# Kernel optimization log

Hardware: AMD Instinct MI355X
Metric: run time of the kernel (lower is better)

## Reference

```python
import jax, jax.numpy as jnp
import numpy as np

C = 512
B, H, W = 4, 64, 64
GROUPS = 32
EPS = 1e-6
SCALE = 1.0 / np.sqrt(C)


def setup_inputs() -> dict:
    key = jax.random.key(0)
    ks = jax.random.split(key, 3)
    x = jax.random.normal(ks[0], (B, C, H, W), dtype=jnp.float32)
    # conv weights: kaiming-ish small init for numerical sanity
    qkv_w = jax.random.normal(ks[1], (3 * C, C), dtype=jnp.float32) * (1.0 / np.sqrt(C))
    proj_w = jax.random.normal(ks[2], (C, C), dtype=jnp.float32) * (1.0 / np.sqrt(C))
    return {
        "x": x,
        "norm_w": jnp.ones((C,), jnp.float32),
        "norm_b": jnp.zeros((C,), jnp.float32),
        "qkv_w": qkv_w,
        "qkv_b": jnp.zeros((3 * C,), jnp.float32),
        "proj_w": proj_w,
        "proj_b": jnp.zeros((C,), jnp.float32),
    }


def reference(x, norm_w, norm_b, qkv_w, qkv_b, proj_w, proj_b):
    b, c, h, w = x.shape
    hw = h * w
    # GroupNorm(32, eps=1e-6, affine)
    xg = x.reshape(b, GROUPS, -1)                       # [B, G, (C/G)*H*W]
    mean = jnp.mean(xg, axis=-1, keepdims=True)
    var = jnp.var(xg, axis=-1, keepdims=True)
    xn = ((xg - mean) * jax.lax.rsqrt(var + EPS)).reshape(b, c, h, w)
    xn = xn * norm_w[:, None, None] + norm_b[:, None, None]
    # 1x1 conv qkv == channel matmul
    qkv = jnp.einsum('oc,bchw->bohw', qkv_w, xn) + qkv_b[:, None, None]
    q, k, v = jnp.split(qkv, 3, axis=1)                 # each [B, C, H, W]
    q = q.reshape(b, c, hw)                              # [B, C, HW]
    k = k.reshape(b, c, hw)
    v = v.reshape(b, c, hw)
    # attn[b, i, j] = softmax_j( q_i . k_j * scale )
    scores = jnp.einsum('bci,bcj->bij', q, k) * SCALE    # [B, HW, HW]
    attn = jax.nn.softmax(scores, axis=-1)
    # h[b, c, i] = sum_j v[b, c, j] * attn[b, i, j]
    hmap = jnp.einsum('bcj,bij->bci', v, attn).reshape(b, c, h, w)
    out = x + jnp.einsum('oc,bchw->bohw', proj_w, hmap) + proj_b[:, None, None]
    return out
```

## Files before the change

kernel.cpp:

```cpp
#include <hip/hip_runtime.h>
#include <hip/hip_fp8.h>
#include <cstdint>
#include <cmath>

#define B_   4
#define C_   512
#define HW_  4096
#define G_   32
#define CPG_ 16
#define EPS_ 1e-6f
#define SCALE_ 0.04419417382415922f
#define PSCALE_ 0.0625f


typedef __bf16 bf16_t;
typedef __bf16 bf16x8 __attribute__((ext_vector_type(8)));
typedef __bf16 bf16x4 __attribute__((ext_vector_type(4)));
typedef float  f32x4  __attribute__((ext_vector_type(4)));
typedef int    i32x4  __attribute__((ext_vector_type(4)));
typedef int    i32x8  __attribute__((ext_vector_type(8)));
typedef unsigned int u32;
typedef __hip_fp8_e4m3 fp8_t;

__device__ __forceinline__ void cp16(const void* g, void* l) {
  __builtin_amdgcn_global_load_lds((__attribute__((address_space(1))) u32*)(g),
                                   (__attribute__((address_space(3))) u32*)(l),
                                   16, 0, 0);
}

__device__ __forceinline__ void zero_acc(f32x4 acc[4][4]) {
  f32x4 z = {0.f, 0.f, 0.f, 0.f};
#pragma unroll
  for (int i = 0; i < 4; ++i)
#pragma unroll
    for (int j = 0; j < 4; ++j) acc[i][j] = z;
}

__device__ __forceinline__ void gemm_bt64(const bf16_t* __restrict__ A,
                                          const bf16_t* __restrict__ B,
                                          int K, int lda, int ldb,
                                          f32x4 acc[4][4]) {
  __shared__ __align__(16) bf16_t As[128 * 64];
  __shared__ __align__(16) bf16_t Bs[128 * 64];
  const int tid  = threadIdx.x;
  const int wave = tid >> 6;
  const int lane = tid & 63;
  const int wm = (wave >> 1) * 64;
  const int wn = (wave & 1) * 64;
  const int srow = lane >> 3;
  const int gch  = ((lane & 7) - srow) & 7;
  const bf16_t* gA = A + (size_t)(wave * 32 + srow) * lda + gch * 8;
  const bf16_t* gB = B + (size_t)(wave * 32 + srow) * ldb + gch * 8;
  bf16_t* lA = As + wave * 32 * 64;
  bf16_t* lB = Bs + wave * 32 * 64;
  const int fr = lane & 15;
  const int q  = lane >> 4;
  const int eo0 = ((q + fr) & 7) * 8;
  const int eo1 = ((q + 4 + fr) & 7) * 8;

  for (int k0 = 0; k0 < K; k0 += 64) {
#pragma unroll
    for (int cc = 0; cc < 4; ++cc) {
      cp16(gA + (size_t)(cc * 8) * lda, lA + cc * 512);
      cp16(gB + (size_t)(cc * 8) * ldb, lB + cc * 512);
    }
    gA += 64; gB += 64;
    __syncthreads();
#pragma unroll
    for (int h = 0; h < 2; ++h) {
      const int eo = h ? eo1 : eo0;
      bf16x8 a[4], b[4];
#pragma unroll
      for (int i = 0; i < 4; ++i)
        a[i] = *(const bf16x8*)(As + (wm + i * 16 + fr) * 64 + eo);
#pragma unroll
      for (int j = 0; j < 4; ++j)
        b[j] = *(const bf16x8*)(Bs + (wn + j * 16 + fr) * 64 + eo);
#pragma unroll
      for (int i = 0; i < 4; ++i)
#pragma unroll
        for (int j = 0; j < 4; ++j)
          acc[i][j] = __builtin_amdgcn_mfma_f32_16x16x32_bf16(a[i], b[j], acc[i][j], 0, 0, 0);
    }
    __syncthreads();
  }
}

template <bool ROWSUM>
__device__ __forceinline__ void gemm_bt_mx(const unsigned char* __restrict__ A,
                                           const unsigned char* __restrict__ B,
                                           int K, int lda, int ldb,
                                           f32x4 acc[4][4], f32x4 accl[4]) {
  __shared__ __align__(16) unsigned char As[128 * 128];
  __shared__ __align__(16) unsigned char Bs[128 * 128];
  const int tid  = threadIdx.x;
  const int wave = tid >> 6;
  const int lane = tid & 63;
  const int wm = (wave >> 1) * 64;
  const int wn = (wave & 1) * 64;
  const int srow = lane >> 3;
  const int gch  = ((lane & 7) - srow) & 7;
  const unsigned char* gA = A + (size_t)(wave * 32 + srow) * lda + gch * 16;
  const unsigned char* gB = B + (size_t)(wave * 32 + srow) * ldb + gch * 16;
  unsigned char* lA = As + wave * 32 * 128;
  unsigned char* lB = Bs + wave * 32 * 128;
  const int fr = lane & 15;
  const int q  = lane >> 4;
  const int co0 = ((2 * q     + fr) & 7) * 16;
  const int co1 = ((2 * q + 1 + fr) & 7) * 16;
  const i32x8 vones = {0x38383838, 0x38383838, 0x38383838, 0x38383838,
                       0x38383838, 0x38383838, 0x38383838, 0x38383838};

  for (int k0 = 0; k0 < K; k0 += 128) {
#pragma unroll
    for (int cc = 0; cc < 4; ++cc) {
      cp16(gA + (size_t)(cc * 8) * lda, lA + cc * 1024);
      cp16(gB + (size_t)(cc * 8) * ldb, lB + cc * 1024);
    }
    gA += 128; gB += 128;
    __syncthreads();
    i32x8 a[4], b[4];
#pragma unroll
    for (int i = 0; i < 4; ++i) {
      const int ro = (wm + i * 16 + fr) * 128;
      i32x4 lo = *(const i32x4*)(As + ro + co0);
      i32x4 hi = *(const i32x4*)(As + ro + co1);
      a[i] = __builtin_shufflevector(lo, hi, 0, 1, 2, 3, 4, 5, 6, 7);
    }
#pragma unroll
    for (int j = 0; j < 4; ++j) {
      const int ro = (wn + j * 16 + fr) * 128;
      i32x4 lo = *(const i32x4*)(Bs + ro + co0);
      i32x4 hi = *(const i32x4*)(Bs + ro + co1);
      b[j] = __builtin_shufflevector(lo, hi, 0, 1, 2, 3, 4, 5, 6, 7);
    }
#pragma unroll
    for (int i = 0; i < 4; ++i) {
#pragma unroll
      for (int j = 0; j < 4; ++j)
        acc[i][j] = __builtin_amdgcn_mfma_scale_f32_16x16x128_f8f6f4(
            a[i], b[j], acc[i][j], 0, 0, 0, 0x7F, 0, 0x7F);
      if (ROWSUM)
        accl[i] = __builtin_amdgcn_mfma_scale_f32_16x16x128_f8f6f4(
            a[i], vones, accl[i], 0, 0, 0, 0x7F, 0, 0x7F);
    }
    __syncthreads();
  }
}


__global__ void __launch_bounds__(256) cast_w_kernel(const float* __restrict__ qkv_w,
                                                     const float* __restrict__ proj_w,
                                                     bf16_t* __restrict__ wqkv,
                                                     bf16_t* __restrict__ wproj) {
  int idx = blockIdx.x * 256 + threadIdx.x;
  const int nq = 1536 * 512;
  if (idx < nq) {
    wqkv[idx] = (bf16_t)qkv_w[idx];
  } else {
    int t = idx - nq;
    int p = t & 511;
    int off = p & 63;
    int c = (p & ~63) + ((off & 3) << 4) + (off >> 2);
    wproj[t] = (bf16_t)proj_w[(t & ~511) + c];
  }
}

__global__ void __launch_bounds__(256) gn_partial_kernel(const float* __restrict__ x,
                                                         float* __restrict__ stats) {
  __shared__ float rs[256], rss[256];
  const int bg = blockIdx.x >> 3;
  const int ch = blockIdx.x & 7;
  const float4* base = (const float4*)(x + (size_t)bg * (CPG_ * HW_)) +
                       (size_t)ch * (CPG_ * HW_ / 4 / 8);
  float s = 0.f, ss = 0.f;
  for (int i = threadIdx.x; i < CPG_ * HW_ / 4 / 8; i += 256) {
    float4 v = base[i];
    s  += v.x + v.y + v.z + v.w;
    ss += v.x * v.x + v.y * v.y + v.z * v.z + v.w * v.w;
  }
  rs[threadIdx.x] = s; rss[threadIdx.x] = ss;
  __syncthreads();
  for (int st = 128; st > 0; st >>= 1) {
    if ((int)threadIdx.x < st) {
      rs[threadIdx.x]  += rs[threadIdx.x + st];
      rss[threadIdx.x] += rss[threadIdx.x + st];
    }
    __syncthreads();
  }
  if (threadIdx.x == 0) {
    atomicAdd(&stats[bg * 2 + 0], rs[0]);
    atomicAdd(&stats[bg * 2 + 1], rss[0]);
  }
}

__global__ void __launch_bounds__(256) norm_tr_kernel(const float* __restrict__ x,
                                                      const float* __restrict__ stats,
                                                      const float* __restrict__ nw,
                                                      const float* __restrict__ nb,
                                                      bf16_t* __restrict__ xnT) {
  __shared__ float tile[64][65];
  const int b  = blockIdx.z;
  const int i0 = blockIdx.x * 64;
  const int c0 = blockIdx.y * 64;
  const int tx = threadIdx.x & 63;
  const int ty = threadIdx.x >> 6;
  const int cbase = c0 + ty * 16;
  const int g = cbase >> 4;
  const float inv = 1.f / (float)(CPG_ * HW_);
  const float sum  = stats[(b * G_ + g) * 2 + 0];
  const float ssum = stats[(b * G_ + g) * 2 + 1];
  const float mean = sum * inv;
  const float rstd = rsqrtf(ssum * inv - mean * mean + EPS_);
#pragma unroll
  for (int r = 0; r < 16; ++r) {
    const int c = cbase + r;
    float v = x[((size_t)b * C_ + c) * HW_ + i0 + tx];
    tile[ty * 16 + r][tx] = (v - mean) * rstd * nw[c] + nb[c];
  }
  __syncthreads();
#pragma unroll
  for (int r = 0; r < 16; ++r) {
    const int il = ty * 16 + r;
    xnT[((size_t)b * HW_ + i0 + il) * C_ + c0 + tx] = (bf16_t)tile[tx][il];
  }
}


__global__ void __launch_bounds__(256) qk_gemm_kernel(const bf16_t* __restrict__ xnT,
                                                      const bf16_t* __restrict__ wqkv,
                                                      const float* __restrict__ qkv_b,
                                                      fp8_t* __restrict__ QKt8) {
  const int b = blockIdx.z;
  f32x4 acc[4][4]; zero_acc(acc);
  const bf16_t* A  = xnT + ((size_t)b * HW_ + blockIdx.y * 128) * C_;
  const bf16_t* Bp = wqkv + (size_t)blockIdx.x * 128 * C_;
  gemm_bt64(A, Bp, C_, C_, C_, acc);
  const int lane = threadIdx.x & 63, wave = threadIdx.x >> 6;
  const int wm = (wave >> 1) * 64, wn = (wave & 1) * 64;
  const int fr = lane & 15, q = lane >> 4;
  const int r0 = blockIdx.y * 128 + wm + (q << 2);
  const int cb = blockIdx.x * 128 + wn;
  float bias[4];
#pragma unroll
  for (int j = 0; j < 4; ++j) bias[j] = qkv_b[cb + fr + j * 16];
#pragma unroll
  for (int i = 0; i < 4; ++i)
#pragma unroll
    for (int r = 0; r < 4; ++r) {
      const int row = r0 + i * 16 + r;
      u32 dw = 0;
      dw = (u32)__builtin_amdgcn_cvt_pk_fp8_f32(acc[i][0][r] + bias[0],
                                                acc[i][1][r] + bias[1], (int)dw, false);
      dw = (u32)__builtin_amdgcn_cvt_pk_fp8_f32(acc[i][2][r] + bias[2],
                                                acc[i][3][r] + bias[3], (int)dw, true);
      *(u32*)((unsigned char*)QKt8 + ((size_t)b * HW_ + row) * 1024 + cb + fr * 4) = dw;
    }
}

__global__ void __launch_bounds__(256) v_gemm_kernel(const bf16_t* __restrict__ wqkv,
                                                     const bf16_t* __restrict__ xnT,
                                                     const float* __restrict__ qkv_b,
                                                     fp8_t* __restrict__ V8) {
  const int b = blockIdx.z;
  f32x4 acc[4][4]; zero_acc(acc);
  const bf16_t* A  = wqkv + (size_t)(1024 + blockIdx.y * 128) * C_;
  const bf16_t* Bp = xnT + ((size_t)b * HW_ + blockIdx.x * 128) * C_;
  gemm_bt64(A, Bp, C_, C_, C_, acc);
  const int lane = threadIdx.x & 63, wave = threadIdx.x >> 6;
  const int wm = (wave >> 1) * 64, wn = (wave & 1) * 64;
  const int fr = lane & 15, q = lane >> 4;
  const int r0 = blockIdx.y * 128 + wm + (q << 2);
  const int cb = blockIdx.x * 128 + wn;
#pragma unroll
  for (int i = 0; i < 4; ++i)
#pragma unroll
    for (int r = 0; r < 4; ++r) {
      const int row = r0 + i * 16 + r;
      const float bias = qkv_b[1024 + row];
      u32 dw = 0;
      dw = (u32)__builtin_amdgcn_cvt_pk_fp8_f32(acc[i][0][r] + bias,
                                                acc[i][1][r] + bias, (int)dw, false);
      dw = (u32)__builtin_amdgcn_cvt_pk_fp8_f32(acc[i][2][r] + bias,
                                                acc[i][3][r] + bias, (int)dw, true);
      *(u32*)((unsigned char*)V8 + ((size_t)b * C_ + row) * HW_ + cb + fr * 4) = dw;
    }
}

__global__ void __launch_bounds__(256) sexp_gemm_kernel(const fp8_t* __restrict__ QKt8,
                                                        fp8_t* __restrict__ P8) {
  const int n   = blockIdx.x;
  const int xcd = n & 7;
  const int p   = n >> 3;
  const int xb  = p & 31;
  const int grp = xcd * 16 + (p >> 5);
  const int yb  = grp & 31;
  const int b   = grp >> 5;

  const unsigned char* QKtb = (const unsigned char*)QKt8 + (size_t)b * HW_ * 1024;
  fp8_t* Pb = P8 + (size_t)b * HW_ * HW_;
  f32x4 acc[4][4]; zero_acc(acc);
  const unsigned char* A  = QKtb + (size_t)yb * 128 * 1024;
  const unsigned char* Bp = QKtb + 512 + (size_t)xb * 128 * 1024;
  gemm_bt_mx<false>(A, Bp, 512, 1024, 1024, acc, nullptr);
  const int lane = threadIdx.x & 63, wave = threadIdx.x >> 6;
  const int wm = (wave >> 1) * 64, wn = (wave & 1) * 64;
  const int fr = lane & 15, q = lane >> 4;
  const int r0 = yb * 128 + wm + (q << 2);
  const int cb = xb * 128 + wn;
#pragma unroll
  for (int i = 0; i < 4; ++i)
#pragma unroll
    for (int r = 0; r < 4; ++r) {
      const int row = r0 + i * 16 + r;
      float e0 = __expf(acc[i][0][r] * SCALE_) * PSCALE_;
      float e1 = __expf(acc[i][1][r] * SCALE_) * PSCALE_;
      float e2 = __expf(acc[i][2][r] * SCALE_) * PSCALE_;
      float e3 = __expf(acc[i][3][r] * SCALE_) * PSCALE_;
      u32 dw = 0;
      dw = (u32)__builtin_amdgcn_cvt_pk_fp8_f32(e0, e1, (int)dw, false);
      dw = (u32)__builtin_amdgcn_cvt_pk_fp8_f32(e2, e3, (int)dw, true);
      *(u32*)((unsigned char*)Pb + (size_t)row * HW_ + cb + fr * 4) = dw;
    }
}

__global__ void __launch_bounds__(256) pv_gemm_kernel(const fp8_t* __restrict__ P8,
                                                      const fp8_t* __restrict__ V8,
                                                      bf16_t* __restrict__ hmT) {
  const int n   = blockIdx.x;
  const int xcd = n & 7;
  const int p   = n >> 3;
  const int xb  = p & 3;
  const int grp = xcd * 16 + (p >> 2);
  const int yb  = grp & 31;
  const int b   = grp >> 5;

  const unsigned char* A  = (const unsigned char*)P8 + (size_t)b * HW_ * HW_ +
                            (size_t)yb * 128 * HW_;
  const unsigned char* Bp = (const unsigned char*)V8 + (size_t)b * C_ * HW_ +
                            (size_t)xb * 128 * HW_;
  bf16_t* hmTb = hmT + (size_t)b * HW_ * C_;

  f32x4 acc[4][4]; zero_acc(acc);
  f32x4 accl[4];
  {
    f32x4 z = {0.f, 0.f, 0.f, 0.f};
#pragma unroll
    for (int i = 0; i < 4; ++i) accl[i] = z;
  }
  gemm_bt_mx<true>(A, Bp, HW_, HW_, HW_, acc, accl);

  const int lane = threadIdx.x & 63, wave = threadIdx.x >> 6;
  const int wm = (wave >> 1) * 64, wn = (wave & 1) * 64;
  const int fr = lane & 15, q = lane >> 4;
  const int r0 = yb * 128 + wm + (q << 2);
  const int cb = xb * 128 + wn;
#pragma unroll
  for (int i = 0; i < 4; ++i)
#pragma unroll
    for (int r = 0; r < 4; ++r) {
      const int row = r0 + i * 16 + r;
      const float rl = 1.f / accl[i][r];
      bf16x4 o;
#pragma unroll
      for (int j = 0; j < 4; ++j) o[j] = (bf16_t)(acc[i][j][r] * rl);
      *(bf16x4*)(hmTb + (size_t)row * C_ + cb + fr * 4) = o;
    }
}

__global__ void __launch_bounds__(256) proj_gemm_kernel(const bf16_t* __restrict__ wproj,
                                                        const bf16_t* __restrict__ hmT,
                                                        const float* __restrict__ proj_b,
                                                        const float* __restrict__ x,
                                                        float* __restrict__ out) {
  const int b = blockIdx.z;
  f32x4 acc[4][4]; zero_acc(acc);
  const bf16_t* A  = wproj + (size_t)blockIdx.y * 128 * C_;
  const bf16_t* Bp = hmT + ((size_t)b * HW_ + blockIdx.x * 128) * C_;
  gemm_bt64(A, Bp, C_, C_, C_, acc);
  const int lane = threadIdx.x & 63, wave = threadIdx.x >> 6;
  const int wm = (wave >> 1) * 64, wn = (wave & 1) * 64;
  const int r0 = blockIdx.y * 128 + wm + ((lane >> 4) << 2);
  const int c0 = blockIdx.x * 128 + wn + (lane & 15);
#pragma unroll
  for (int i = 0; i < 4; ++i)
#pragma unroll
    for (int r = 0; r < 4; ++r) {
      const int row = r0 + i * 16 + r;
      const float bias = proj_b[row];
#pragma unroll
      for (int j = 0; j < 4; ++j) {
        const int col = c0 + j * 16;
        const size_t idx = ((size_t)b * C_ + row) * HW_ + col;
        out[idx] = x[idx] + bias + acc[i][j][r];
      }
    }
}

extern "C" void kernel_launch(void* const* d_in, const int* in_sizes, int n_in,
                              void* d_out, int out_size, void* d_ws, size_t ws_size,
                              hipStream_t stream) {
  const float* x      = (const float*)d_in[0];
  const float* norm_w = (const float*)d_in[1];
  const float* norm_b = (const float*)d_in[2];
  const float* qkv_w  = (const float*)d_in[3];
  const float* qkv_b  = (const float*)d_in[4];
  const float* proj_w = (const float*)d_in[5];
  const float* proj_b = (const float*)d_in[6];
  float* out = (float*)d_out;

  char* ws = (char*)d_ws;
  size_t o = 0;
  bf16_t* wqkv  = (bf16_t*)(ws + o); o += (size_t)1536 * 512 * 2;
  bf16_t* wproj = (bf16_t*)(ws + o); o += (size_t)512 * 512 * 2;
  float*  stats = (float*)(ws + o);  o += 128 * 2 * 4;
  bf16_t* xnT   = (bf16_t*)(ws + o); o += (size_t)B_ * HW_ * C_ * 2;
  fp8_t*  QKt8  = (fp8_t*)(ws + o);  o += (size_t)B_ * HW_ * 1024;
  fp8_t*  V8    = (fp8_t*)(ws + o);  o += (size_t)B_ * C_ * HW_;
  bf16_t* hmT   = (bf16_t*)(ws + o); o += (size_t)B_ * HW_ * C_ * 2;
  fp8_t*  P8    = (fp8_t*)(ws + o);  o += (size_t)B_ * HW_ * HW_;

  cast_w_kernel<<<4096, 256, 0, stream>>>(qkv_w, proj_w, wqkv, wproj);
  hipMemsetAsync(stats, 0, 128 * 2 * sizeof(float), stream);
  gn_partial_kernel<<<1024, 256, 0, stream>>>(x, stats);
  norm_tr_kernel<<<dim3(HW_ / 64, C_ / 64, B_), 256, 0, stream>>>(x, stats, norm_w, norm_b, xnT);
  qk_gemm_kernel<<<dim3(1024 / 128, HW_ / 128, B_), 256, 0, stream>>>(xnT, wqkv, qkv_b, QKt8);
  v_gemm_kernel<<<dim3(HW_ / 128, C_ / 128, B_), 256, 0, stream>>>(wqkv, xnT, qkv_b, V8);
  sexp_gemm_kernel<<<4096, 256, 0, stream>>>(QKt8, P8);
  pv_gemm_kernel<<<512, 256, 0, stream>>>(P8, V8, hmT);
  proj_gemm_kernel<<<dim3(HW_ / 128, C_ / 128, B_), 256, 0, stream>>>(
      wproj, hmT, proj_b, x, out);
}
```

Before: 247.8 us.

## Convert QKV, V and projection GEMMs from bf16 to scaled fp8 MFMA

Weights, the normalized input and the attention output are now stored as fp8 e4m3 instead of bf16. Weights and hmap are pre-scaled by 16, and the MFMA scale exponents (0x7B) undo that factor. The three 512-deep GEMMs (QK, V, proj) now use the fp8 scaled MFMA path instead of bf16 MFMA, which halves their global and LDS traffic and doubles MFMA throughput. The cost is lower precision in the projections and the residual-path GEMM, which may hurt accuracy.

```diff
diff --git a/kernel.cpp b/kernel.cpp
--- a/kernel.cpp
+++ b/kernel.cpp
@@ -15,7 +15,6 @@
 
 typedef __bf16 bf16_t;
 typedef __bf16 bf16x8 __attribute__((ext_vector_type(8)));
-typedef __bf16 bf16x4 __attribute__((ext_vector_type(4)));
 typedef float  f32x4  __attribute__((ext_vector_type(4)));
 typedef int    i32x4  __attribute__((ext_vector_type(4)));
 typedef int    i32x8  __attribute__((ext_vector_type(8)));
@@ -36,57 +35,7 @@
     for (int j = 0; j < 4; ++j) acc[i][j] = z;
 }
 
-__device__ __forceinline__ void gemm_bt64(const bf16_t* __restrict__ A,
-                                          const bf16_t* __restrict__ B,
-                                          int K, int lda, int ldb,
-                                          f32x4 acc[4][4]) {
-  __shared__ __align__(16) bf16_t As[128 * 64];
-  __shared__ __align__(16) bf16_t Bs[128 * 64];
-  const int tid  = threadIdx.x;
-  const int wave = tid >> 6;
-  const int lane = tid & 63;
-  const int wm = (wave >> 1) * 64;
-  const int wn = (wave & 1) * 64;
-  const int srow = lane >> 3;
-  const int gch  = ((lane & 7) - srow) & 7;
-  const bf16_t* gA = A + (size_t)(wave * 32 + srow) * lda + gch * 8;
-  const bf16_t* gB = B + (size_t)(wave * 32 + srow) * ldb + gch * 8;
-  bf16_t* lA = As + wave * 32 * 64;
-  bf16_t* lB = Bs + wave * 32 * 64;
-  const int fr = lane & 15;
-  const int q  = lane >> 4;
-  const int eo0 = ((q + fr) & 7) * 8;
-  const int eo1 = ((q + 4 + fr) & 7) * 8;
-
-  for (int k0 = 0; k0 < K; k0 += 64) {
-#pragma unroll
-    for (int cc = 0; cc < 4; ++cc) {
-      cp16(gA + (size_t)(cc * 8) * lda, lA + cc * 512);
-      cp16(gB + (size_t)(cc * 8) * ldb, lB + cc * 512);
-    }
-    gA += 64; gB += 64;
-    __syncthreads();
-#pragma unroll
-    for (int h = 0; h < 2; ++h) {
-      const int eo = h ? eo1 : eo0;
-      bf16x8 a[4], b[4];
-#pragma unroll
-      for (int i = 0; i < 4; ++i)
-        a[i] = *(const bf16x8*)(As + (wm + i * 16 + fr) * 64 + eo);
-#pragma unroll
-      for (int j = 0; j < 4; ++j)
-        b[j] = *(const bf16x8*)(Bs + (wn + j * 16 + fr) * 64 + eo);
-#pragma unroll
-      for (int i = 0; i < 4; ++i)
-#pragma unroll
-        for (int j = 0; j < 4; ++j)
-          acc[i][j] = __builtin_amdgcn_mfma_f32_16x16x32_bf16(a[i], b[j], acc[i][j], 0, 0, 0);
-    }
-    __syncthreads();
-  }
-}
-
-template <bool ROWSUM>
+template <bool ROWSUM, int SA = 0x7F, int SB = 0x7F>
 __device__ __forceinline__ void gemm_bt_mx(const unsigned char* __restrict__ A,
                                            const unsigned char* __restrict__ B,
                                            int K, int lda, int ldb,
@@ -139,10 +88,10 @@
 #pragma unroll
       for (int j = 0; j < 4; ++j)
         acc[i][j] = __builtin_amdgcn_mfma_scale_f32_16x16x128_f8f6f4(
-            a[i], b[j], acc[i][j], 0, 0, 0, 0x7F, 0, 0x7F);
+            a[i], b[j], acc[i][j], 0, 0, 0, SA, 0, SB);
       if (ROWSUM)
         accl[i] = __builtin_amdgcn_mfma_scale_f32_16x16x128_f8f6f4(
-            a[i], vones, accl[i], 0, 0, 0, 0x7F, 0, 0x7F);
+            a[i], vones, accl[i], 0, 0, 0, SA, 0, 0x7F);
     }
     __syncthreads();
   }
@@ -151,18 +100,32 @@
 
 __global__ void __launch_bounds__(256) cast_w_kernel(const float* __restrict__ qkv_w,
                                                      const float* __restrict__ proj_w,
-                                                     bf16_t* __restrict__ wqkv,
-                                                     bf16_t* __restrict__ wproj) {
-  int idx = blockIdx.x * 256 + threadIdx.x;
+                                                     fp8_t* __restrict__ wqkv8,
+                                                     fp8_t* __restrict__ wproj8) {
+  const int idx = blockIdx.x * 256 + threadIdx.x;
+  const int t = idx * 4;
   const int nq = 1536 * 512;
-  if (idx < nq) {
-    wqkv[idx] = (bf16_t)qkv_w[idx];
+  if (t < nq) {
+    u32 dw = 0;
+    dw = (u32)__builtin_amdgcn_cvt_pk_fp8_f32(qkv_w[t] * 16.f, qkv_w[t + 1] * 16.f, (int)dw, false);
+    dw = (u32)__builtin_amdgcn_cvt_pk_fp8_f32(qkv_w[t + 2] * 16.f, qkv_w[t + 3] * 16.f, (int)dw, true);
+    *(u32*)((unsigned char*)wqkv8 + t) = dw;
   } else {
-    int t = idx - nq;
-    int p = t & 511;
-    int off = p & 63;
-    int c = (p & ~63) + ((off & 3) << 4) + (off >> 2);
-    wproj[t] = (bf16_t)proj_w[(t & ~511) + c];
+    const int tt = t - nq;
+    const int o = tt >> 9;
+    const int p = tt & 511;
+    float v[4];
+#pragma unroll
+    for (int e = 0; e < 4; ++e) {
+      const int pe = p + e;
+      const int off = pe & 63;
+      const int c = (pe & ~63) + ((off & 3) << 4) + (off >> 2);
+      v[e] = proj_w[(o << 9) + c] * 16.f;
+    }
+    u32 dw = 0;
+    dw = (u32)__builtin_amdgcn_cvt_pk_fp8_f32(v[0], v[1], (int)dw, false);
+    dw = (u32)__builtin_amdgcn_cvt_pk_fp8_f32(v[2], v[3], (int)dw, true);
+    *(u32*)((unsigned char*)wproj8 + tt) = dw;
   }
 }
 
@@ -198,7 +161,7 @@
                                                       const float* __restrict__ stats,
                                                       const float* __restrict__ nw,
                                                       const float* __restrict__ nb,
-                                                      bf16_t* __restrict__ xnT) {
+                                                      fp8_t* __restrict__ xnT8) {
   __shared__ float tile[64][65];
   const int b  = blockIdx.z;
   const int i0 = blockIdx.x * 64;
@@ -219,23 +182,28 @@
     tile[ty * 16 + r][tx] = (v - mean) * rstd * nw[c] + nb[c];
   }
   __syncthreads();
-#pragma unroll
-  for (int r = 0; r < 16; ++r) {
-    const int il = ty * 16 + r;
-    xnT[((size_t)b * HW_ + i0 + il) * C_ + c0 + tx] = (bf16_t)tile[tx][il];
-  }
-}
-
-
-__global__ void __launch_bounds__(256) qk_gemm_kernel(const bf16_t* __restrict__ xnT,
-                                                      const bf16_t* __restrict__ wqkv,
+  const int il = threadIdx.x >> 2;
+  const int q4 = threadIdx.x & 3;
+#pragma unroll
+  for (int m = 0; m < 4; ++m) {
+    const int cq = q4 + m * 4;
+    u32 dw = 0;
+    dw = (u32)__builtin_amdgcn_cvt_pk_fp8_f32(tile[cq * 4 + 0][il], tile[cq * 4 + 1][il], (int)dw, false);
+    dw = (u32)__builtin_amdgcn_cvt_pk_fp8_f32(tile[cq * 4 + 2][il], tile[cq * 4 + 3][il], (int)dw, true);
+    *(u32*)((unsigned char*)xnT8 + ((size_t)b * HW_ + i0 + il) * C_ + c0 + cq * 4) = dw;
+  }
+}
+
+
+__global__ void __launch_bounds__(256) qk_gemm_kernel(const fp8_t* __restrict__ xnT8,
+                                                      const fp8_t* __restrict__ wqkv8,
                                                       const float* __restrict__ qkv_b,
                                                       fp8_t* __restrict__ QKt8) {
   const int b = blockIdx.z;
   f32x4 acc[4][4]; zero_acc(acc);
-  const bf16_t* A  = xnT + ((size_t)b * HW_ + blockIdx.y * 128) * C_;
-  const bf16_t* Bp = wqkv + (size_t)blockIdx.x * 128 * C_;
-  gemm_bt64(A, Bp, C_, C_, C_, acc);
+  const unsigned char* A  = (const unsigned char*)xnT8 + ((size_t)b * HW_ + blockIdx.y * 128) * C_;
+  const unsigned char* Bp = (const unsigned char*)wqkv8 + (size_t)blockIdx.x * 128 * C_;
+  gemm_bt_mx<false, 0x7F, 0x7B>(A, Bp, C_, C_, C_, acc, nullptr);
   const int lane = threadIdx.x & 63, wave = threadIdx.x >> 6;
   const int wm = (wave >> 1) * 64, wn = (wave & 1) * 64;
   const int fr = lane & 15, q = lane >> 4;
@@ -258,15 +226,15 @@
     }
 }
 
-__global__ void __launch_bounds__(256) v_gemm_kernel(const bf16_t* __restrict__ wqkv,
-                                                     const bf16_t* __restrict__ xnT,
+__global__ void __launch_bounds__(256) v_gemm_kernel(const fp8_t* __restrict__ wqkv8,
+                                                     const fp8_t* __restrict__ xnT8,
                                                      const float* __restrict__ qkv_b,
                                                      fp8_t* __restrict__ V8) {
   const int b = blockIdx.z;
   f32x4 acc[4][4]; zero_acc(acc);
-  const bf16_t* A  = wqkv + (size_t)(1024 + blockIdx.y * 128) * C_;
-  const bf16_t* Bp = xnT + ((size_t)b * HW_ + blockIdx.x * 128) * C_;
-  gemm_bt64(A, Bp, C_, C_, C_, acc);
+  const unsigned char* A  = (const unsigned char*)wqkv8 + (size_t)(1024 + blockIdx.y * 128) * C_;
+  const unsigned char* Bp = (const unsigned char*)xnT8 + ((size_t)b * HW_ + blockIdx.x * 128) * C_;
+  gemm_bt_mx<false, 0x7B, 0x7F>(A, Bp, C_, C_, C_, acc, nullptr);
   const int lane = threadIdx.x & 63, wave = threadIdx.x >> 6;
   const int wm = (wave >> 1) * 64, wn = (wave & 1) * 64;
   const int fr = lane & 15, q = lane >> 4;
@@ -326,7 +294,7 @@
 
 __global__ void __launch_bounds__(256) pv_gemm_kernel(const fp8_t* __restrict__ P8,
                                                       const fp8_t* __restrict__ V8,
-                                                      bf16_t* __restrict__ hmT) {
+                                                      fp8_t* __restrict__ hmT8) {
   const int n   = blockIdx.x;
   const int xcd = n & 7;
   const int p   = n >> 3;
@@ -339,7 +307,7 @@
                             (size_t)yb * 128 * HW_;
   const unsigned char* Bp = (const unsigned char*)V8 + (size_t)b * C_ * HW_ +
                             (size_t)xb * 128 * HW_;
-  bf16_t* hmTb = hmT + (size_t)b * HW_ * C_;
+  fp8_t* hmTb = hmT8 + (size_t)b * HW_ * C_;
 
   f32x4 acc[4][4]; zero_acc(acc);
   f32x4 accl[4];
@@ -360,24 +328,24 @@
 #pragma unroll
     for (int r = 0; r < 4; ++r) {
       const int row = r0 + i * 16 + r;
-      const float rl = 1.f / accl[i][r];
-      bf16x4 o;
-#pragma unroll
-      for (int j = 0; j < 4; ++j) o[j] = (bf16_t)(acc[i][j][r] * rl);
-      *(bf16x4*)(hmTb + (size_t)row * C_ + cb + fr * 4) = o;
-    }
-}
-
-__global__ void __launch_bounds__(256) proj_gemm_kernel(const bf16_t* __restrict__ wproj,
-                                                        const bf16_t* __restrict__ hmT,
+      const float rl = 16.f / accl[i][r];
+      u32 dw = 0;
+      dw = (u32)__builtin_amdgcn_cvt_pk_fp8_f32(acc[i][0][r] * rl, acc[i][1][r] * rl, (int)dw, false);
+      dw = (u32)__builtin_amdgcn_cvt_pk_fp8_f32(acc[i][2][r] * rl, acc[i][3][r] * rl, (int)dw, true);
+      *(u32*)((unsigned char*)hmTb + (size_t)row * C_ + cb + fr * 4) = dw;
+    }
+}
+
+__global__ void __launch_bounds__(256) proj_gemm_kernel(const fp8_t* __restrict__ wproj8,
+                                                        const fp8_t* __restrict__ hmT8,
                                                         const float* __restrict__ proj_b,
                                                         const float* __restrict__ x,
                                                         float* __restrict__ out) {
   const int b = blockIdx.z;
   f32x4 acc[4][4]; zero_acc(acc);
-  const bf16_t* A  = wproj + (size_t)blockIdx.y * 128 * C_;
-  const bf16_t* Bp = hmT + ((size_t)b * HW_ + blockIdx.x * 128) * C_;
-  gemm_bt64(A, Bp, C_, C_, C_, acc);
+  const unsigned char* A  = (const unsigned char*)wproj8 + (size_t)blockIdx.y * 128 * C_;
+  const unsigned char* Bp = (const unsigned char*)hmT8 + ((size_t)b * HW_ + blockIdx.x * 128) * C_;
+  gemm_bt_mx<false, 0x7B, 0x7B>(A, Bp, C_, C_, C_, acc, nullptr);
   const int lane = threadIdx.x & 63, wave = threadIdx.x >> 6;
   const int wm = (wave >> 1) * 64, wn = (wave & 1) * 64;
   const int r0 = blockIdx.y * 128 + wm + ((lane >> 4) << 2);
@@ -411,23 +379,23 @@
 
   char* ws = (char*)d_ws;
   size_t o = 0;
-  bf16_t* wqkv  = (bf16_t*)(ws + o); o += (size_t)1536 * 512 * 2;
-  bf16_t* wproj = (bf16_t*)(ws + o); o += (size_t)512 * 512 * 2;
-  float*  stats = (float*)(ws + o);  o += 128 * 2 * 4;
-  bf16_t* xnT   = (bf16_t*)(ws + o); o += (size_t)B_ * HW_ * C_ * 2;
-  fp8_t*  QKt8  = (fp8_t*)(ws + o);  o += (size_t)B_ * HW_ * 1024;
-  fp8_t*  V8    = (fp8_t*)(ws + o);  o += (size_t)B_ * C_ * HW_;
-  bf16_t* hmT   = (bf16_t*)(ws + o); o += (size_t)B_ * HW_ * C_ * 2;
-  fp8_t*  P8    = (fp8_t*)(ws + o);  o += (size_t)B_ * HW_ * HW_;
-
-  cast_w_kernel<<<4096, 256, 0, stream>>>(qkv_w, proj_w, wqkv, wproj);
+  fp8_t* wqkv8  = (fp8_t*)(ws + o); o += (size_t)1536 * 512;
+  fp8_t* wproj8 = (fp8_t*)(ws + o); o += (size_t)512 * 512;
+  float* stats  = (float*)(ws + o); o += 128 * 2 * 4;
+  fp8_t* xnT8   = (fp8_t*)(ws + o); o += (size_t)B_ * HW_ * C_;
+  fp8_t* QKt8   = (fp8_t*)(ws + o); o += (size_t)B_ * HW_ * 1024;
+  fp8_t* V8     = (fp8_t*)(ws + o); o += (size_t)B_ * C_ * HW_;
+  fp8_t* hmT8   = (fp8_t*)(ws + o); o += (size_t)B_ * HW_ * C_;
+  fp8_t* P8     = (fp8_t*)(ws + o); o += (size_t)B_ * HW_ * HW_;
+
+  cast_w_kernel<<<1024, 256, 0, stream>>>(qkv_w, proj_w, wqkv8, wproj8);
   hipMemsetAsync(stats, 0, 128 * 2 * sizeof(float), stream);
   gn_partial_kernel<<<1024, 256, 0, stream>>>(x, stats);
-  norm_tr_kernel<<<dim3(HW_ / 64, C_ / 64, B_), 256, 0, stream>>>(x, stats, norm_w, norm_b, xnT);
-  qk_gemm_kernel<<<dim3(1024 / 128, HW_ / 128, B_), 256, 0, stream>>>(xnT, wqkv, qkv_b, QKt8);
-  v_gemm_kernel<<<dim3(HW_ / 128, C_ / 128, B_), 256, 0, stream>>>(wqkv, xnT, qkv_b, V8);
+  norm_tr_kernel<<<dim3(HW_ / 64, C_ / 64, B_), 256, 0, stream>>>(x, stats, norm_w, norm_b, xnT8);
+  qk_gemm_kernel<<<dim3(1024 / 128, HW_ / 128, B_), 256, 0, stream>>>(xnT8, wqkv8, qkv_b, QKt8);
+  v_gemm_kernel<<<dim3(HW_ / 128, C_ / 128, B_), 256, 0, stream>>>(wqkv8, xnT8, qkv_b, V8);
   sexp_gemm_kernel<<<4096, 256, 0, stream>>>(QKt8, P8);
-  pv_gemm_kernel<<<512, 256, 0, stream>>>(P8, V8, hmT);
+  pv_gemm_kernel<<<512, 256, 0, stream>>>(P8, V8, hmT8);
   proj_gemm_kernel<<<dim3(HW_ / 128, C_ / 128, B_), 256, 0, stream>>>(
-      wproj, hmT, proj_b, x, out);
-}
+      wproj8, hmT8, proj_b, x, out);
+}
```

Measured after the change: 239.5 us. 1.03x faster.
